# Performance work log

Hardware: AMD Instinct MI355X
Metric: run time of the kernel (lower is better)

The kernel has to match this reference:

```python
import jax, jax.numpy as jnp
import numpy as np

NUM_LINKS = 1048576


def _euler_rots(theta):
    # theta: [N,3] -> per-link rotation R = Rz @ Ry @ Rx, shape [N,3,3]
    cx, cy, cz = jnp.cos(theta[:, 0]), jnp.cos(theta[:, 1]), jnp.cos(theta[:, 2])
    sx, sy, sz = jnp.sin(theta[:, 0]), jnp.sin(theta[:, 1]), jnp.sin(theta[:, 2])
    z = jnp.zeros_like(cx)
    o = jnp.ones_like(cx)
    rx = jnp.stack([jnp.stack([o, z, z], -1),
                    jnp.stack([z, cx, -sx], -1),
                    jnp.stack([z, sx, cx], -1)], -2)
    ry = jnp.stack([jnp.stack([cy, z, sy], -1),
                    jnp.stack([z, o, z], -1),
                    jnp.stack([-sy, z, cy], -1)], -2)
    rz = jnp.stack([jnp.stack([cz, -sz, z], -1),
                    jnp.stack([sz, cz, z], -1),
                    jnp.stack([z, z, o], -1)], -2)
    return jnp.matmul(rz, jnp.matmul(ry, rx))  # [N,3,3]


def setup_inputs() -> dict:
    key = jax.random.key(0)
    k1, k2 = jax.random.split(key)
    link_lengths = jax.random.uniform(k1, (NUM_LINKS,), dtype=jnp.float32)
    theta = jax.random.normal(k2, (NUM_LINKS, 3), dtype=jnp.float32)
    return {"link_lengths": link_lengths, "theta": theta}


def reference(link_lengths, theta):
    # Original loop computes eff_pos_i = sum_{j=0..i} (R_0 @ R_1 @ ... @ R_j) @ t_j
    # with t_j = l_j * e_z. Vectorize via prefix matrix products + cumsum.
    R = _euler_rots(theta)                                   # [N,3,3]
    P = jax.lax.associative_scan(jnp.matmul, R)              # P_j = R_0@...@R_j
    v = P[:, :, 2] * link_lengths[:, None]                   # P_j @ (l_j * e_z)
    return jnp.cumsum(v, axis=0)                             # [N,3]
```

## Files before the change

kernel.cpp:

```cpp
#include <hip/hip_runtime.h>
#include <math.h>


#define K1_TPB 512
#define K1_EPT 2
#define K1_EPB (K1_TPB * K1_EPT)
#define K1_NW (K1_TPB / 64)
#define K2_TPB 256
#define K2_EPT 4
#define K2_EPB (K2_TPB * K2_EPT)
#define K2_NW (K2_TPB / 64)
#define MAXB 1024
#define EPG (MAXB / K2_TPB)

struct Xf {
    float m[9];
    float p[3];
};

__device__ __forceinline__ void xf_identity(Xf& x) {
    x.m[0] = 1.f; x.m[1] = 0.f; x.m[2] = 0.f;
    x.m[3] = 0.f; x.m[4] = 1.f; x.m[5] = 0.f;
    x.m[6] = 0.f; x.m[7] = 0.f; x.m[8] = 1.f;
    x.p[0] = 0.f; x.p[1] = 0.f; x.p[2] = 0.f;
}

__device__ __forceinline__ Xf xf_comb(const Xf& A, const Xf& B) {
    Xf o;
#pragma unroll
    for (int r = 0; r < 3; ++r) {
        const float a0 = A.m[r * 3 + 0], a1 = A.m[r * 3 + 1], a2 = A.m[r * 3 + 2];
#pragma unroll
        for (int c = 0; c < 3; ++c) {
            o.m[r * 3 + c] = a0 * B.m[0 * 3 + c] + a1 * B.m[1 * 3 + c] + a2 * B.m[2 * 3 + c];
        }
        o.p[r] = A.p[r] + a0 * B.p[0] + a1 * B.p[1] + a2 * B.p[2];
    }
    return o;
}

__device__ __forceinline__ void fast_sincos(float x, float& s, float& c) {
    const float fn = __builtin_rintf(x * 0.636619772367581343f);
    const int n = (int)fn;
    float r = __builtin_fmaf(fn, -1.57079637050628662109375f, x);
    r = __builtin_fmaf(fn, 4.37113900018624283e-8f, r);
    const float r2 = r * r;
    float sp = __builtin_fmaf(r2, -1.9515295891e-4f, 8.3321608736e-3f);
    sp = __builtin_fmaf(r2, sp, -1.6666654611e-1f);
    const float ss = __builtin_fmaf(r * r2, sp, r);
    float cp = __builtin_fmaf(r2, 2.443315711809948e-5f, -1.388731625493765e-3f);
    cp = __builtin_fmaf(r2, cp, 4.166664568298827e-2f);
    const float cc = __builtin_fmaf(r2 * r2, cp,
                                    __builtin_fmaf(r2, -0.5f, 1.0f));
    const int q = n & 3;
    const float s0 = (q & 1) ? cc : ss;
    const float c0 = (q & 1) ? ss : cc;
    const unsigned sgn_s = (unsigned)(q & 2) << 30;
    const unsigned sgn_c = (unsigned)((q + 1) & 2) << 30;
    s = __uint_as_float(__float_as_uint(s0) ^ sgn_s);
    c = __uint_as_float(__float_as_uint(c0) ^ sgn_c);
}

__device__ __forceinline__ void xf_fold(Xf& a, float ax, float ay, float az, float l) {
    float sx, cx, sy, cy, sz, cz;
    fast_sincos(ax, sx, cx);
    fast_sincos(ay, sy, cy);
    fast_sincos(az, sz, cz);
    const float sysx = sy * sx, sycx = sy * cx;
    const float r00 = cz * cy;
    const float r01 = cz * sysx - sz * cx;
    const float r02 = sz * sx + cz * sycx;
    const float r10 = sz * cy;
    const float r11 = cz * cx + sz * sysx;
    const float r12 = sz * sycx - cz * sx;
    const float r20 = -sy;
    const float r21 = cy * sx;
    const float r22 = cy * cx;
    const float t0 = l * r02, t1 = l * r12, t2 = l * r22;
    const float p0 = a.p[0] + a.m[0] * t0 + a.m[1] * t1 + a.m[2] * t2;
    const float p1 = a.p[1] + a.m[3] * t0 + a.m[4] * t1 + a.m[5] * t2;
    const float p2 = a.p[2] + a.m[6] * t0 + a.m[7] * t1 + a.m[8] * t2;
    const float n0 = a.m[0] * r00 + a.m[1] * r10 + a.m[2] * r20;
    const float n1 = a.m[0] * r01 + a.m[1] * r11 + a.m[2] * r21;
    const float n2 = a.m[0] * r02 + a.m[1] * r12 + a.m[2] * r22;
    const float n3 = a.m[3] * r00 + a.m[4] * r10 + a.m[5] * r20;
    const float n4 = a.m[3] * r01 + a.m[4] * r11 + a.m[5] * r21;
    const float n5 = a.m[3] * r02 + a.m[4] * r12 + a.m[5] * r22;
    const float n6 = a.m[6] * r00 + a.m[7] * r10 + a.m[8] * r20;
    const float n7 = a.m[6] * r01 + a.m[7] * r11 + a.m[8] * r21;
    const float n8 = a.m[6] * r02 + a.m[7] * r12 + a.m[8] * r22;
    a.m[0] = n0; a.m[1] = n1; a.m[2] = n2;
    a.m[3] = n3; a.m[4] = n4; a.m[5] = n5;
    a.m[6] = n6; a.m[7] = n7; a.m[8] = n8;
    a.p[0] = p0; a.p[1] = p1; a.p[2] = p2;
}

template <int CTRL, int RMASK>
__device__ __forceinline__ float dpp_f(float src, float oldv) {
    return __int_as_float(__builtin_amdgcn_update_dpp(
        __float_as_int(oldv), __float_as_int(src), CTRL, RMASK, 0xF, false));
}

template <int CTRL, int RMASK>
__device__ __forceinline__ Xf xf_scan_step(const Xf& v) {
    Xf b;
    b.m[0] = dpp_f<CTRL, RMASK>(v.m[0], 1.f);
    b.m[1] = dpp_f<CTRL, RMASK>(v.m[1], 0.f);
    b.m[2] = dpp_f<CTRL, RMASK>(v.m[2], 0.f);
    b.m[3] = dpp_f<CTRL, RMASK>(v.m[3], 0.f);
    b.m[4] = dpp_f<CTRL, RMASK>(v.m[4], 1.f);
    b.m[5] = dpp_f<CTRL, RMASK>(v.m[5], 0.f);
    b.m[6] = dpp_f<CTRL, RMASK>(v.m[6], 0.f);
    b.m[7] = dpp_f<CTRL, RMASK>(v.m[7], 0.f);
    b.m[8] = dpp_f<CTRL, RMASK>(v.m[8], 1.f);
    b.p[0] = dpp_f<CTRL, RMASK>(v.p[0], 0.f);
    b.p[1] = dpp_f<CTRL, RMASK>(v.p[1], 0.f);
    b.p[2] = dpp_f<CTRL, RMASK>(v.p[2], 0.f);
    return xf_comb(b, v);
}

__device__ __forceinline__ Xf wave_scan(Xf v) {
    v = xf_scan_step<0x111, 0xF>(v);
    v = xf_scan_step<0x112, 0xF>(v);
    v = xf_scan_step<0x114, 0xF>(v);
    v = xf_scan_step<0x118, 0xF>(v);
    v = xf_scan_step<0x142, 0xA>(v);
    v = xf_scan_step<0x143, 0xC>(v);
    return v;
}

__device__ __forceinline__ Xf xf_shfl_up1(const Xf& a) {
    Xf o;
#pragma unroll
    for (int k = 0; k < 9; ++k) o.m[k] = __shfl_up(a.m[k], 1, 64);
#pragma unroll
    for (int k = 0; k < 3; ++k) o.p[k] = __shfl_up(a.p[k], 1, 64);
    return o;
}

__device__ __forceinline__ Xf xf_load4(const Xf* p) {
    const float4* g = (const float4*)p;
    const float4 x = g[0], y = g[1], z = g[2];
    Xf b;
    b.m[0] = x.x; b.m[1] = x.y; b.m[2] = x.z;
    b.m[3] = x.w; b.m[4] = y.x; b.m[5] = y.y;
    b.m[6] = y.z; b.m[7] = y.w; b.m[8] = z.x;
    b.p[0] = z.y; b.p[1] = z.z; b.p[2] = z.w;
    return b;
}
__device__ __forceinline__ void xf_store4(Xf* p, const Xf& b) {
    float4* g = (float4*)p;
    g[0] = make_float4(b.m[0], b.m[1], b.m[2], b.m[3]);
    g[1] = make_float4(b.m[4], b.m[5], b.m[6], b.m[7]);
    g[2] = make_float4(b.m[8], b.p[0], b.p[1], b.p[2]);
}

__device__ __forceinline__ void xf_apply(const Xf& T, float q0, float q1, float q2,
                                         float& o0, float& o1, float& o2) {
    o0 = T.p[0] + T.m[0] * q0 + T.m[1] * q1 + T.m[2] * q2;
    o1 = T.p[1] + T.m[3] * q0 + T.m[4] * q1 + T.m[5] * q2;
    o2 = T.p[2] + T.m[6] * q0 + T.m[7] * q1 + T.m[8] * q2;
}

__global__ void __launch_bounds__(K1_TPB, 8)
fk_local(const float* __restrict__ ll, const float* __restrict__ th,
         Xf* __restrict__ agg, float* __restrict__ out, int n) {
    __shared__ Xf wagg[K1_NW];
    const int t = threadIdx.x, bid = blockIdx.x;
    const int lane = t & 63, w = t >> 6;
    const long long j0 = (long long)bid * K1_EPB + (long long)t * K1_EPT;

    Xf a;
    xf_identity(a);
    float pe[K1_EPT][3];
    if (j0 + K1_EPT <= n) {
        const float2* th2 = (const float2*)(th + 3 * j0);
        const float2 d0 = th2[0], d1 = th2[1], d2 = th2[2];
        const float2 L = *(const float2*)(ll + j0);
        xf_fold(a, d0.x, d0.y, d1.x, L.x);
        pe[0][0] = a.p[0]; pe[0][1] = a.p[1]; pe[0][2] = a.p[2];
        xf_fold(a, d1.y, d2.x, d2.y, L.y);
        pe[1][0] = a.p[0]; pe[1][1] = a.p[1]; pe[1][2] = a.p[2];
    } else {
#pragma unroll
        for (int e = 0; e < K1_EPT; ++e) {
            const long long j = j0 + e;
            if (j < n) xf_fold(a, th[3 * j + 0], th[3 * j + 1], th[3 * j + 2], ll[j]);
            pe[e][0] = a.p[0]; pe[e][1] = a.p[1]; pe[e][2] = a.p[2];
        }
    }

    const Xf inc = wave_scan(a);
    if (lane == 63) wagg[w] = inc;
    __syncthreads();

    Xf exw;
    xf_identity(exw);
    for (int k = 0; k < w; ++k) exw = xf_comb(exw, wagg[k]);

    if (t == K1_TPB - 1) xf_store4(&agg[bid], xf_comb(exw, inc));

    const Xf ext = xf_shfl_up1(inc);
    Xf T = exw;
    if (lane != 0) T = xf_comb(T, ext);

    if (j0 + K1_EPT <= n) {
        float o0, o1, o2, o3, o4, o5;
        xf_apply(T, pe[0][0], pe[0][1], pe[0][2], o0, o1, o2);
        xf_apply(T, pe[1][0], pe[1][1], pe[1][2], o3, o4, o5);
        float2* q2 = (float2*)(out + 3 * j0);
        q2[0] = make_float2(o0, o1);
        q2[1] = make_float2(o2, o3);
        q2[2] = make_float2(o4, o5);
    } else {
#pragma unroll
        for (int e = 0; e < K1_EPT; ++e) {
            const long long j = j0 + e;
            if (j < n) {
                float o0, o1, o2;
                xf_apply(T, pe[e][0], pe[e][1], pe[e][2], o0, o1, o2);
                out[3 * j + 0] = o0; out[3 * j + 1] = o1; out[3 * j + 2] = o2;
            }
        }
    }
}

__global__ void __launch_bounds__(K2_TPB, 8)
fk_fixup(const Xf* __restrict__ agg, float* __restrict__ out, int n, int nb) {
    __shared__ Xf wred[K2_NW];
    __shared__ Xf shG;
    const int t = threadIdx.x, bid = blockIdx.x;
    const int lane = t & 63, w = t >> 6;

    {
        const int i0 = t * EPG;
        Xf A;
        xf_identity(A);
#pragma unroll
        for (int e = 0; e < EPG; ++e) {
            const int i = i0 + e;
            if (i < bid) A = xf_comb(A, xf_load4(&agg[i]));
        }
        const Xf inc = wave_scan(A);
        if (lane == 63) wred[w] = inc;
    }
    __syncthreads();
    if (t == 0) {
        Xf G = wred[0];
#pragma unroll
        for (int k = 1; k < K2_NW; ++k) G = xf_comb(G, wred[k]);
        shG = G;
    }
    __syncthreads();
    const Xf G = shG;

    const long long j0 = (long long)bid * K2_EPB + (long long)t * K2_EPT;
    if (j0 + K2_EPT <= n) {
        float4* o4 = (float4*)(out + 3 * j0);
        const float4 x = o4[0], y = o4[1], z = o4[2];
        float r[12];
        xf_apply(G, x.x, x.y, x.z, r[0], r[1], r[2]);
        xf_apply(G, x.w, y.x, y.y, r[3], r[4], r[5]);
        xf_apply(G, y.z, y.w, z.x, r[6], r[7], r[8]);
        xf_apply(G, z.y, z.z, z.w, r[9], r[10], r[11]);
        o4[0] = make_float4(r[0], r[1], r[2], r[3]);
        o4[1] = make_float4(r[4], r[5], r[6], r[7]);
        o4[2] = make_float4(r[8], r[9], r[10], r[11]);
    } else {
#pragma unroll
        for (int e = 0; e < K2_EPT; ++e) {
            const long long j = j0 + e;
            if (j < n) {
                float o0, o1, o2;
                xf_apply(G, out[3 * j + 0], out[3 * j + 1], out[3 * j + 2], o0, o1, o2);
                out[3 * j + 0] = o0; out[3 * j + 1] = o1; out[3 * j + 2] = o2;
            }
        }
    }
}

extern "C" void kernel_launch(void* const* d_in, const int* in_sizes, int n_in,
                              void* d_out, int out_size, void* d_ws, size_t ws_size,
                              hipStream_t stream) {
    const float* ll = (const float*)d_in[0];
    const float* th = (const float*)d_in[1];
    float* out = (float*)d_out;
    const int n = in_sizes[0];

    int nb = (n + K1_EPB - 1) / K1_EPB;
    if (nb > MAXB) nb = MAXB;

    Xf* agg = (Xf*)d_ws;

    fk_local<<<nb, K1_TPB, 0, stream>>>(ll, th, agg, out, n);
    fk_fixup<<<nb, K2_TPB, 0, stream>>>(agg, out, n, nb);
}
```

Baseline: 33.01 us.

## Use one element per thread with smaller scan blocks and decoupled fixup grid

The first kernel now gives each thread one link instead of folding two serially. Blocks shrink to 256 threads, so there are up to 4096 block aggregates. The in-block scan result is applied directly, which removes the lane shift-up and the extra combine. The fixup kernel now spans several scan blocks per block: each quarter of the block folds in the extra preceding aggregates it needs, and the aggregate reduction is split into two independent chains. The aim is more parallelism and shorter serial dependency chains, at the cost of more aggregates to reduce in the fixup pass (8 loads per thread).

```diff
diff --git a/kernel.cpp b/kernel.cpp
--- a/kernel.cpp
+++ b/kernel.cpp
@@ -2,16 +2,15 @@
 #include <math.h>
 
 
-#define K1_TPB 512
-#define K1_EPT 2
-#define K1_EPB (K1_TPB * K1_EPT)
+#define K1_TPB 256
 #define K1_NW (K1_TPB / 64)
-#define K2_TPB 256
-#define K2_EPT 4
+#define K2_TPB 512
+#define K2_EPT 2
 #define K2_EPB (K2_TPB * K2_EPT)
 #define K2_NW (K2_TPB / 64)
-#define MAXB 1024
-#define EPG (MAXB / K2_TPB)
+#define RATIO (K2_EPB / K1_TPB)
+#define MAXB1 4096
+#define EPG (MAXB1 / K2_TPB)
 
 struct Xf {
     float m[9];
@@ -61,38 +60,24 @@
     c = __uint_as_float(__float_as_uint(c0) ^ sgn_c);
 }
 
-__device__ __forceinline__ void xf_fold(Xf& a, float ax, float ay, float az, float l) {
+__device__ __forceinline__ void xf_elem(Xf& a, float ax, float ay, float az, float l) {
     float sx, cx, sy, cy, sz, cz;
     fast_sincos(ax, sx, cx);
     fast_sincos(ay, sy, cy);
     fast_sincos(az, sz, cz);
     const float sysx = sy * sx, sycx = sy * cx;
-    const float r00 = cz * cy;
-    const float r01 = cz * sysx - sz * cx;
-    const float r02 = sz * sx + cz * sycx;
-    const float r10 = sz * cy;
-    const float r11 = cz * cx + sz * sysx;
-    const float r12 = sz * sycx - cz * sx;
-    const float r20 = -sy;
-    const float r21 = cy * sx;
-    const float r22 = cy * cx;
-    const float t0 = l * r02, t1 = l * r12, t2 = l * r22;
-    const float p0 = a.p[0] + a.m[0] * t0 + a.m[1] * t1 + a.m[2] * t2;
-    const float p1 = a.p[1] + a.m[3] * t0 + a.m[4] * t1 + a.m[5] * t2;
-    const float p2 = a.p[2] + a.m[6] * t0 + a.m[7] * t1 + a.m[8] * t2;
-    const float n0 = a.m[0] * r00 + a.m[1] * r10 + a.m[2] * r20;
-    const float n1 = a.m[0] * r01 + a.m[1] * r11 + a.m[2] * r21;
-    const float n2 = a.m[0] * r02 + a.m[1] * r12 + a.m[2] * r22;
-    const float n3 = a.m[3] * r00 + a.m[4] * r10 + a.m[5] * r20;
-    const float n4 = a.m[3] * r01 + a.m[4] * r11 + a.m[5] * r21;
-    const float n5 = a.m[3] * r02 + a.m[4] * r12 + a.m[5] * r22;
-    const float n6 = a.m[6] * r00 + a.m[7] * r10 + a.m[8] * r20;
-    const float n7 = a.m[6] * r01 + a.m[7] * r11 + a.m[8] * r21;
-    const float n8 = a.m[6] * r02 + a.m[7] * r12 + a.m[8] * r22;
-    a.m[0] = n0; a.m[1] = n1; a.m[2] = n2;
-    a.m[3] = n3; a.m[4] = n4; a.m[5] = n5;
-    a.m[6] = n6; a.m[7] = n7; a.m[8] = n8;
-    a.p[0] = p0; a.p[1] = p1; a.p[2] = p2;
+    a.m[0] = cz * cy;
+    a.m[1] = cz * sysx - sz * cx;
+    a.m[2] = sz * sx + cz * sycx;
+    a.m[3] = sz * cy;
+    a.m[4] = cz * cx + sz * sysx;
+    a.m[5] = sz * sycx - cz * sx;
+    a.m[6] = -sy;
+    a.m[7] = cy * sx;
+    a.m[8] = cy * cx;
+    a.p[0] = l * a.m[2];
+    a.p[1] = l * a.m[5];
+    a.p[2] = l * a.m[8];
 }
 
 template <int CTRL, int RMASK>
@@ -129,15 +114,6 @@
     return v;
 }
 
-__device__ __forceinline__ Xf xf_shfl_up1(const Xf& a) {
-    Xf o;
-#pragma unroll
-    for (int k = 0; k < 9; ++k) o.m[k] = __shfl_up(a.m[k], 1, 64);
-#pragma unroll
-    for (int k = 0; k < 3; ++k) o.p[k] = __shfl_up(a.p[k], 1, 64);
-    return o;
-}
-
 __device__ __forceinline__ Xf xf_load4(const Xf* p) {
     const float4* g = (const float4*)p;
     const float4 x = g[0], y = g[1], z = g[2];
@@ -163,31 +139,18 @@
 }
 
 __global__ void __launch_bounds__(K1_TPB, 8)
-fk_local(const float* __restrict__ ll, const float* __restrict__ th,
+fk_scan1(const float* __restrict__ ll, const float* __restrict__ th,
          Xf* __restrict__ agg, float* __restrict__ out, int n) {
     __shared__ Xf wagg[K1_NW];
     const int t = threadIdx.x, bid = blockIdx.x;
     const int lane = t & 63, w = t >> 6;
-    const long long j0 = (long long)bid * K1_EPB + (long long)t * K1_EPT;
+    const long long j = (long long)bid * K1_TPB + t;
 
     Xf a;
-    xf_identity(a);
-    float pe[K1_EPT][3];
-    if (j0 + K1_EPT <= n) {
-        const float2* th2 = (const float2*)(th + 3 * j0);
-        const float2 d0 = th2[0], d1 = th2[1], d2 = th2[2];
-        const float2 L = *(const float2*)(ll + j0);
-        xf_fold(a, d0.x, d0.y, d1.x, L.x);
-        pe[0][0] = a.p[0]; pe[0][1] = a.p[1]; pe[0][2] = a.p[2];
-        xf_fold(a, d1.y, d2.x, d2.y, L.y);
-        pe[1][0] = a.p[0]; pe[1][1] = a.p[1]; pe[1][2] = a.p[2];
+    if (j < n) {
+        xf_elem(a, th[3 * j + 0], th[3 * j + 1], th[3 * j + 2], ll[j]);
     } else {
-#pragma unroll
-        for (int e = 0; e < K1_EPT; ++e) {
-            const long long j = j0 + e;
-            if (j < n) xf_fold(a, th[3 * j + 0], th[3 * j + 1], th[3 * j + 2], ll[j]);
-            pe[e][0] = a.p[0]; pe[e][1] = a.p[1]; pe[e][2] = a.p[2];
-        }
+        xf_identity(a);
     }
 
     const Xf inc = wave_scan(a);
@@ -200,47 +163,40 @@
 
     if (t == K1_TPB - 1) xf_store4(&agg[bid], xf_comb(exw, inc));
 
-    const Xf ext = xf_shfl_up1(inc);
-    Xf T = exw;
-    if (lane != 0) T = xf_comb(T, ext);
-
-    if (j0 + K1_EPT <= n) {
-        float o0, o1, o2, o3, o4, o5;
-        xf_apply(T, pe[0][0], pe[0][1], pe[0][2], o0, o1, o2);
-        xf_apply(T, pe[1][0], pe[1][1], pe[1][2], o3, o4, o5);
-        float2* q2 = (float2*)(out + 3 * j0);
-        q2[0] = make_float2(o0, o1);
-        q2[1] = make_float2(o2, o3);
-        q2[2] = make_float2(o4, o5);
-    } else {
-#pragma unroll
-        for (int e = 0; e < K1_EPT; ++e) {
-            const long long j = j0 + e;
-            if (j < n) {
-                float o0, o1, o2;
-                xf_apply(T, pe[e][0], pe[e][1], pe[e][2], o0, o1, o2);
-                out[3 * j + 0] = o0; out[3 * j + 1] = o1; out[3 * j + 2] = o2;
-            }
-        }
-    }
-}
-
-__global__ void __launch_bounds__(K2_TPB, 8)
-fk_fixup(const Xf* __restrict__ agg, float* __restrict__ out, int n, int nb) {
+    if (j < n) {
+        float q0, q1, q2;
+        xf_apply(exw, inc.p[0], inc.p[1], inc.p[2], q0, q1, q2);
+        out[3 * j + 0] = q0;
+        out[3 * j + 1] = q1;
+        out[3 * j + 2] = q2;
+    }
+}
+
+__global__ void __launch_bounds__(K2_TPB, 4)
+fk_fixup(const Xf* __restrict__ agg, float* __restrict__ out, int n, int nagg) {
     __shared__ Xf wred[K2_NW];
     __shared__ Xf shG;
     const int t = threadIdx.x, bid = blockIdx.x;
     const int lane = t & 63, w = t >> 6;
+    const int base = bid * RATIO;
+    const int lim = base < nagg ? base : nagg;
 
     {
         const int i0 = t * EPG;
-        Xf A;
-        xf_identity(A);
-#pragma unroll
-        for (int e = 0; e < EPG; ++e) {
+        Xf A1, A2;
+        xf_identity(A1);
+        xf_identity(A2);
+#pragma unroll
+        for (int e = 0; e < EPG / 2; ++e) {
             const int i = i0 + e;
-            if (i < bid) A = xf_comb(A, xf_load4(&agg[i]));
-        }
+            if (i < lim) A1 = xf_comb(A1, xf_load4(&agg[i]));
+        }
+#pragma unroll
+        for (int e = EPG / 2; e < EPG; ++e) {
+            const int i = i0 + e;
+            if (i < lim) A2 = xf_comb(A2, xf_load4(&agg[i]));
+        }
+        const Xf A = xf_comb(A1, A2);
         const Xf inc = wave_scan(A);
         if (lane == 63) wred[w] = inc;
     }
@@ -252,28 +208,32 @@
         shG = G;
     }
     __syncthreads();
-    const Xf G = shG;
+
+    const int qd = t >> 7;
+    Xf Gs = shG;
+#pragma unroll
+    for (int k = 0; k < RATIO - 1; ++k) {
+        if (k < qd && base + k < nagg) Gs = xf_comb(Gs, xf_load4(&agg[base + k]));
+    }
 
     const long long j0 = (long long)bid * K2_EPB + (long long)t * K2_EPT;
     if (j0 + K2_EPT <= n) {
-        float4* o4 = (float4*)(out + 3 * j0);
-        const float4 x = o4[0], y = o4[1], z = o4[2];
-        float r[12];
-        xf_apply(G, x.x, x.y, x.z, r[0], r[1], r[2]);
-        xf_apply(G, x.w, y.x, y.y, r[3], r[4], r[5]);
-        xf_apply(G, y.z, y.w, z.x, r[6], r[7], r[8]);
-        xf_apply(G, z.y, z.z, z.w, r[9], r[10], r[11]);
-        o4[0] = make_float4(r[0], r[1], r[2], r[3]);
-        o4[1] = make_float4(r[4], r[5], r[6], r[7]);
-        o4[2] = make_float4(r[8], r[9], r[10], r[11]);
+        float2* o2 = (float2*)(out + 3 * j0);
+        const float2 x = o2[0], y = o2[1], z = o2[2];
+        float r0, r1, r2, r3, r4, r5;
+        xf_apply(Gs, x.x, x.y, y.x, r0, r1, r2);
+        xf_apply(Gs, y.y, z.x, z.y, r3, r4, r5);
+        o2[0] = make_float2(r0, r1);
+        o2[1] = make_float2(r2, r3);
+        o2[2] = make_float2(r4, r5);
     } else {
 #pragma unroll
         for (int e = 0; e < K2_EPT; ++e) {
             const long long j = j0 + e;
             if (j < n) {
-                float o0, o1, o2;
-                xf_apply(G, out[3 * j + 0], out[3 * j + 1], out[3 * j + 2], o0, o1, o2);
-                out[3 * j + 0] = o0; out[3 * j + 1] = o1; out[3 * j + 2] = o2;
+                float o0, o1, o2v;
+                xf_apply(Gs, out[3 * j + 0], out[3 * j + 1], out[3 * j + 2], o0, o1, o2v);
+                out[3 * j + 0] = o0; out[3 * j + 1] = o1; out[3 * j + 2] = o2v;
             }
         }
     }
@@ -287,11 +247,12 @@
     float* out = (float*)d_out;
     const int n = in_sizes[0];
 
-    int nb = (n + K1_EPB - 1) / K1_EPB;
-    if (nb > MAXB) nb = MAXB;
+    int nb1 = (n + K1_TPB - 1) / K1_TPB;
+    if (nb1 > MAXB1) nb1 = MAXB1;
+    int nb2 = (n + K2_EPB - 1) / K2_EPB;
 
     Xf* agg = (Xf*)d_ws;
 
-    fk_local<<<nb, K1_TPB, 0, stream>>>(ll, th, agg, out, n);
-    fk_fixup<<<nb, K2_TPB, 0, stream>>>(agg, out, n, nb);
-}
+    fk_scan1<<<nb1, K1_TPB, 0, stream>>>(ll, th, agg, out, n);
+    fk_fixup<<<nb2, K2_TPB, 0, stream>>>(agg, out, n, nb1);
+}
```

Result: slower. 47.26 us (+43.1%).
